# Optimization experiments

Measured on AMD Instinct MI355X. Metric: run time of the kernel, lower is better.

## Reference

```python
import jax, jax.numpy as jnp
import numpy as np

N = 50000      # nodes
E = 800000     # edges (avg degree 16)
CIN = 64       # in_channels
COUT = 128     # hidden_channels (block out_channels)
TC = 512       # time_channels = 4*hidden
H = 4          # attention heads
DH = COUT // H # head dim
G = 8          # group-norm groups
SLOPE = 0.01   # LeakyReLU default slope


def group_norm(x, w, b, groups=G, eps=1e-5):
    n, c = x.shape
    xg = x.reshape(n, groups, c // groups)
    mu = xg.mean(-1, keepdims=True)
    var = xg.var(-1, keepdims=True)
    xn = ((xg - mu) * jax.lax.rsqrt(var + eps)).reshape(n, c)
    return xn * w + b


def gcn_conv(x, W, b, row, col, ew, n):
    # GCNConv: add self loops (weight 1), symmetric normalization
    sl = jnp.arange(n)
    r = jnp.concatenate([row, sl])
    c = jnp.concatenate([col, sl])
    w2 = jnp.concatenate([ew, jnp.ones((n,), ew.dtype)])
    deg = jax.ops.segment_sum(w2, c, num_segments=n)
    dinv = jnp.where(deg > 0, jax.lax.rsqrt(deg), 0.0)
    norm = dinv[r] * w2 * dinv[c]            # [E+N]
    xw = x @ W                                # [N, Cout]
    out = jax.ops.segment_sum(norm[:, None] * xw[r], c, num_segments=n)
    return out + b


def gat_conv(x, Wa, a_src, a_dst, a_edge, ba, row, col, ew, n):
    # GAT-style attention conv; self-loop edge weight filled with max(edge_weight)
    sl = jnp.arange(n)
    fill = ew.max()
    r = jnp.concatenate([row, sl])
    c = jnp.concatenate([col, sl])
    w2 = jnp.concatenate([ew, jnp.full((n,), fill, ew.dtype)])
    h = (x @ Wa).reshape(n, H, DH)            # [N, H, DH]
    al_s = (h * a_src).sum(-1)                # [N, H]
    al_d = (h * a_dst).sum(-1)                # [N, H]
    logits = jax.nn.leaky_relu(al_s[r] + al_d[c] + a_edge * w2[:, None], 0.2)
    m = jax.ops.segment_max(logits, c, num_segments=n)
    e = jnp.exp(logits - m[c])
    s = jax.ops.segment_sum(e, c, num_segments=n)
    alpha = e / (s[c] + 1e-16)                # [E+N, H]
    out = jax.ops.segment_sum(alpha[:, :, None] * h[r], c, num_segments=n)
    return out.reshape(n, H * DH) + ba


def setup_inputs() -> dict:
    key = jax.random.key(0)
    ks = jax.random.split(key, 24)
    def w(k, shape, fan_in):
        return (jax.random.normal(k, shape, jnp.float32) / np.sqrt(fan_in)).astype(jnp.float32)
    inp = {
        "x": jax.random.normal(ks[0], (N, CIN), jnp.float32),
        "t": jax.random.normal(ks[1], (TC,), jnp.float32),
        "edge_index": jax.random.randint(ks[2], (2, E), 0, N, jnp.int32),
        "edge_weight": jax.random.uniform(ks[3], (E,), jnp.float32),
        # ResBlock norm/conv params
        "gn0_w": jnp.ones((CIN,), jnp.float32), "gn0_b": jnp.zeros((CIN,), jnp.float32),
        "W1": w(ks[4], (CIN, COUT), CIN), "b1": jnp.zeros((COUT,), jnp.float32),
        "gn1_w": jnp.ones((COUT,), jnp.float32), "gn1_b": jnp.zeros((COUT,), jnp.float32),
        "W2": w(ks[5], (COUT, COUT), COUT), "b2": jnp.zeros((COUT,), jnp.float32),
        "Wres": w(ks[6], (CIN, COUT), CIN),
        "te_w": w(ks[7], (TC, COUT), TC), "te_b": jnp.zeros((COUT,), jnp.float32),
        # AttnBlock params
        "gn2_w": jnp.ones((COUT,), jnp.float32), "gn2_b": jnp.zeros((COUT,), jnp.float32),
        "Wa": w(ks[8], (COUT, H * DH), COUT),
        "a_src": w(ks[9], (H, DH), DH), "a_dst": w(ks[10], (H, DH), DH),
        "a_edge": w(ks[11], (H,), 1), "ba": jnp.zeros((H * DH,), jnp.float32),
    }
    return inp


def reference(x, t, edge_index, edge_weight,
              gn0_w, gn0_b, W1, b1, gn1_w, gn1_b, W2, b2, Wres, te_w, te_b,
              gn2_w, gn2_b, Wa, a_src, a_dst, a_edge, ba):
    row, col = edge_index[0], edge_index[1]
    leaky = lambda z: jax.nn.leaky_relu(z, SLOPE)
    # ResBlock (n_layers=2)
    h = gcn_conv(leaky(group_norm(x, gn0_w, gn0_b)), W1, b1, row, col, edge_weight, N)
    tt = leaky(t) @ te_w + te_b               # time embed, broadcasts over nodes
    h = h + tt
    h = gcn_conv(leaky(group_norm(h, gn1_w, gn1_b)), W2, b2, row, col, edge_weight, N)
    h = h + x @ Wres                          # residual (Cin != Cout -> Linear)
    # AttnBlock (n_layers=1)
    a = leaky(group_norm(h, gn2_w, gn2_b))
    out = gat_conv(a, Wa, a_src, a_dst, a_edge, ba, row, col, edge_weight, N)
    return out
```

## Files before the change

### kernel.cpp

```cpp
#include <hip/hip_runtime.h>
#include <math.h>

#define ELLW 48
#define FB 4

typedef __attribute__((ext_vector_type(8))) short frag_ab;
typedef __attribute__((ext_vector_type(4))) float frag_cd;

__device__ __forceinline__ float lk(float v, float s) { return v > 0.f ? v : v * s; }
__device__ __forceinline__ unsigned short f2b(float f) {
    unsigned u = __float_as_uint(f);
    return (unsigned short)((u + 0x7fffu + ((u >> 16) & 1u)) >> 16);
}
__device__ __forceinline__ float b2f(unsigned h) { return __uint_as_float(h << 16); }

__global__ __launch_bounds__(256) void k_init(int* cnt, float* tt,
                                              const float* __restrict__ te_b,
                                              const float* __restrict__ b1, int n) {
    int i = blockIdx.x * 256 + threadIdx.x;
    if (i < n) cnt[i] = 0;
    if (i < 128) tt[i] = te_b[i] + b1[i];
}

__global__ __launch_bounds__(256) void k_fill_ell(const int* __restrict__ row,
                                                  const int* __restrict__ col,
                                                  const float* __restrict__ ew,
                                                  int* cnt, int2* __restrict__ ell,
                                                  float* __restrict__ bmax, int E) {
    int base = blockIdx.x * (256 * FB);
    int tid = threadIdx.x;
    int r[FB], c[FB]; float w[FB]; bool v[FB];
#pragma unroll
    for (int i = 0; i < FB; ++i) {
        int e = base + i * 256 + tid;
        v[i] = (e < E);
        r[i] = 0; c[i] = 0; w[i] = 0.f;
        if (v[i]) { r[i] = row[e]; c[i] = col[e]; w[i] = ew[e]; }
    }
    int pos[FB];
#pragma unroll
    for (int i = 0; i < FB; ++i)
        if (v[i]) pos[i] = atomicAdd(&cnt[c[i]], 1);
#pragma unroll
    for (int i = 0; i < FB; ++i)
        if (v[i] && pos[i] < ELLW)
            ell[(size_t)c[i] * ELLW + pos[i]] = make_int2(r[i], __float_as_int(w[i]));
    float m = 0.f;
#pragma unroll
    for (int i = 0; i < FB; ++i) m = fmaxf(m, w[i]);
    for (int o = 32; o; o >>= 1) m = fmaxf(m, __shfl_down(m, o, 64));
    __shared__ float sm[4];
    if ((tid & 63) == 0) sm[tid >> 6] = m;
    __syncthreads();
    if (tid == 0) bmax[blockIdx.x] = fmaxf(fmaxf(sm[0], sm[1]), fmaxf(sm[2], sm[3]));
}

__global__ __launch_bounds__(256) void k_ewmax_final(const float* __restrict__ bmax,
                                                     float* __restrict__ fill, int nb) {
    int tid = threadIdx.x;
    float m = 0.f;
    for (int i = tid; i < nb; i += 256) m = fmaxf(m, bmax[i]);
    for (int o = 32; o; o >>= 1) m = fmaxf(m, __shfl_down(m, o, 64));
    __shared__ float sm[4];
    if ((tid & 63) == 0) sm[tid >> 6] = m;
    __syncthreads();
    if (tid == 0) *fill = fmaxf(fmaxf(sm[0], sm[1]), fmaxf(sm[2], sm[3]));
}

__global__ __launch_bounds__(256) void k_node_deg(const int* __restrict__ cnt,
                                                  const int2* __restrict__ ell,
                                                  float* __restrict__ dinv, int n) {
    int i = blockIdx.x * 256 + threadIdx.x;
    if (i >= n) return;
    int c = min(cnt[i], ELLW);
    const int2* p = ell + (size_t)i * ELLW;
    float s = 1.f;
    for (int j = 0; j < c; ++j) s += __int_as_float(p[j].y);
    dinv[i] = rsqrtf(s);
}

__global__ __launch_bounds__(128) void k_tt(const float* __restrict__ t,
                                            const float* __restrict__ te_w, float* tt) {
    int co = threadIdx.x;
    int k0 = blockIdx.x * 32;
    float s = 0.f;
    for (int k = k0; k < k0 + 32; ++k) {
        float tv = t[k]; tv = tv > 0.f ? tv : 0.01f * tv;
        s = fmaf(tv, te_w[k * 128 + co], s);
    }
    unsafeAtomicAdd(&tt[co], s);
}

template <int K>
__global__ __launch_bounds__(256) void k_repack(const float* __restrict__ W, unsigned short* __restrict__ Wp) {
    int i = blockIdx.x * 256 + threadIdx.x;
    if (i >= K * 128) return;
    int k = i >> 7, nn = i & 127;
    int kc = k >> 5, quad = (k >> 3) & 3, j = k & 7;
    Wp[(((size_t)(kc * 4 + quad) * 128) + nn) * 8 + j] = f2b(W[i]);
}

template <int C>
__global__ __launch_bounds__(256) void k_gn(const float* __restrict__ in,
                                            const float* __restrict__ gw,
                                            const float* __restrict__ gb,
                                            unsigned short* __restrict__ outh,
                                            unsigned short* __restrict__ rawh, int n) {
    constexpr int CPG = C / 8;
    int gid = blockIdx.x * 256 + threadIdx.x;
    int row = gid >> 3, g = gid & 7;
    if (row >= n) return;
    const float* p = in + (size_t)row * C + g * CPG;
    float v[CPG];
#pragma unroll
    for (int j = 0; j < CPG; j += 4) {
        float4 t4 = *(const float4*)(p + j);
        v[j] = t4.x; v[j + 1] = t4.y; v[j + 2] = t4.z; v[j + 3] = t4.w;
    }
    float s = 0.f, s2 = 0.f;
#pragma unroll
    for (int j = 0; j < CPG; ++j) { s += v[j]; s2 += v[j] * v[j]; }
    float mu = s * (1.0f / CPG);
    float var = s2 * (1.0f / CPG) - mu * mu;
    float rstd = rsqrtf(var + 1e-5f);
    const float* wj = gw + g * CPG;
    const float* bj = gb + g * CPG;
    unsigned pk[CPG / 2];
#pragma unroll
    for (int j = 0; j < CPG; j += 2) {
        float y0 = lk((v[j + 0] - mu) * rstd * wj[j + 0] + bj[j + 0], 0.01f);
        float y1 = lk((v[j + 1] - mu) * rstd * wj[j + 1] + bj[j + 1], 0.01f);
        pk[j / 2] = (unsigned)f2b(y0) | ((unsigned)f2b(y1) << 16);
    }
    unsigned* q = (unsigned*)(outh + (size_t)row * C + g * CPG);
#pragma unroll
    for (int j = 0; j < CPG / 2; j += 4) *(uint4*)(q + j) = *(uint4*)(pk + j);
    if (rawh) {
#pragma unroll
        for (int j = 0; j < CPG; j += 2)
            pk[j / 2] = (unsigned)f2b(v[j]) | ((unsigned)f2b(v[j + 1]) << 16);
        unsigned* q2 = (unsigned*)(rawh + (size_t)row * C + g * CPG);
#pragma unroll
        for (int j = 0; j < CPG / 2; j += 4) *(uint4*)(q2 + j) = *(uint4*)(pk + j);
    }
}

template <int K>
__global__ __launch_bounds__(256) void k_mgemm(const unsigned short* __restrict__ Xh,
                                               const unsigned short* __restrict__ Wp,
                                               unsigned short* __restrict__ OUTh, int n) {
    int tid = threadIdx.x;
    int wave = tid >> 6, lane = tid & 63;
    int quad = lane >> 4, l16 = lane & 15;
    int rbase = blockIdx.x * 64 + wave * 16;
    int arow = rbase + l16; if (arow >= n) arow = n - 1;
    frag_cd acc[8];
#pragma unroll
    for (int t = 0; t < 8; ++t) acc[t] = (frag_cd){0.f, 0.f, 0.f, 0.f};
    const unsigned short* ap = Xh + (size_t)arow * K + quad * 8;
#pragma unroll
    for (int kc = 0; kc < K / 32; ++kc) {
        frag_ab a = *(const frag_ab*)(ap + kc * 32);
        const unsigned short* bp = Wp + ((size_t)(kc * 4 + quad) * 128 + l16) * 8;
#pragma unroll
        for (int t = 0; t < 8; ++t) {
            frag_ab b = *(const frag_ab*)(bp + (size_t)t * 128);
            acc[t] = __builtin_amdgcn_mfma_f32_16x16x32_bf16(a, b, acc[t], 0, 0, 0);
        }
    }
#pragma unroll
    for (int reg = 0; reg < 4; ++reg) {
        int r = rbase + quad * 4 + reg;
        if (r >= n) continue;
#pragma unroll
        for (int t = 0; t < 8; ++t)
            OUTh[(size_t)r * 128 + t * 16 + l16] = f2b(acc[t][reg]);
    }
}

__global__ __launch_bounds__(256) void k_mgemm2(const unsigned short* __restrict__ X1,
                                                const unsigned short* __restrict__ W2p,
                                                const unsigned short* __restrict__ X2,
                                                const unsigned short* __restrict__ Wrp,
                                                unsigned short* __restrict__ OUTh,
                                                float* __restrict__ C2,
                                                const float* __restrict__ bias, int n) {
    int tid = threadIdx.x;
    int wave = tid >> 6, lane = tid & 63;
    int quad = lane >> 4, l16 = lane & 15;
    int rbase = blockIdx.x * 64 + wave * 16;
    int arow = rbase + l16; if (arow >= n) arow = n - 1;
    frag_cd acc1[8], acc2[8];
#pragma unroll
    for (int t = 0; t < 8; ++t) {
        acc1[t] = (frag_cd){0.f, 0.f, 0.f, 0.f};
        acc2[t] = (frag_cd){0.f, 0.f, 0.f, 0.f};
    }
    const unsigned short* ap1 = X1 + (size_t)arow * 128 + quad * 8;
#pragma unroll
    for (int kc = 0; kc < 4; ++kc) {
        frag_ab a = *(const frag_ab*)(ap1 + kc * 32);
        const unsigned short* bp = W2p + ((size_t)(kc * 4 + quad) * 128 + l16) * 8;
#pragma unroll
        for (int t = 0; t < 8; ++t) {
            frag_ab b = *(const frag_ab*)(bp + (size_t)t * 128);
            acc1[t] = __builtin_amdgcn_mfma_f32_16x16x32_bf16(a, b, acc1[t], 0, 0, 0);
        }
    }
    const unsigned short* ap2 = X2 + (size_t)arow * 64 + quad * 8;
#pragma unroll
    for (int kc = 0; kc < 2; ++kc) {
        frag_ab a = *(const frag_ab*)(ap2 + kc * 32);
        const unsigned short* bp = Wrp + ((size_t)(kc * 4 + quad) * 128 + l16) * 8;
#pragma unroll
        for (int t = 0; t < 8; ++t) {
            frag_ab b = *(const frag_ab*)(bp + (size_t)t * 128);
            acc2[t] = __builtin_amdgcn_mfma_f32_16x16x32_bf16(a, b, acc2[t], 0, 0, 0);
        }
    }
#pragma unroll
    for (int reg = 0; reg < 4; ++reg) {
        int r = rbase + quad * 4 + reg;
        if (r >= n) continue;
#pragma unroll
        for (int t = 0; t < 8; ++t) {
            int c = t * 16 + l16;
            size_t o = (size_t)r * 128 + c;
            OUTh[o] = f2b(acc1[t][reg]);
            C2[o] = bias[c] + acc2[t][reg];
        }
    }
}

template <int BASEVEC>
__global__ __launch_bounds__(256) void k_gather_gn(const int* __restrict__ cnt,
                                                   const int2* __restrict__ ell,
                                                   const float* __restrict__ dinv,
                                                   const unsigned short* __restrict__ Bh,
                                                   const float* __restrict__ basevec,
                                                   const float* __restrict__ basebuf,
                                                   const float* __restrict__ gw,
                                                   const float* __restrict__ gb,
                                                   unsigned short* __restrict__ outh, int n) {
    int gid = blockIdx.x * 256 + threadIdx.x;
    int node = gid >> 5, q = gid & 31;
    if (node >= n) return;
    int s = node * ELLW;
    int e2 = s + min(cnt[node], ELLW);
    float a0 = 0.f, a1 = 0.f, a2 = 0.f, a3 = 0.f;
    int j = s;
    for (; j + 4 <= e2; j += 4) {
        int2 p0 = ell[j], p1 = ell[j + 1], p2 = ell[j + 2], p3 = ell[j + 3];
        float d0 = dinv[p0.x], d1 = dinv[p1.x], d2 = dinv[p2.x], d3 = dinv[p3.x];
        uint2 v0 = *(const uint2*)(Bh + (size_t)p0.x * 128 + q * 4);
        uint2 v1 = *(const uint2*)(Bh + (size_t)p1.x * 128 + q * 4);
        uint2 v2 = *(const uint2*)(Bh + (size_t)p2.x * 128 + q * 4);
        uint2 v3 = *(const uint2*)(Bh + (size_t)p3.x * 128 + q * 4);
        float w0 = d0 * __int_as_float(p0.y), w1 = d1 * __int_as_float(p1.y);
        float w2 = d2 * __int_as_float(p2.y), w3 = d3 * __int_as_float(p3.y);
        a0 = fmaf(w0, b2f(v0.x & 0xffffu), a0); a1 = fmaf(w0, b2f(v0.x >> 16), a1);
        a2 = fmaf(w0, b2f(v0.y & 0xffffu), a2); a3 = fmaf(w0, b2f(v0.y >> 16), a3);
        a0 = fmaf(w1, b2f(v1.x & 0xffffu), a0); a1 = fmaf(w1, b2f(v1.x >> 16), a1);
        a2 = fmaf(w1, b2f(v1.y & 0xffffu), a2); a3 = fmaf(w1, b2f(v1.y >> 16), a3);
        a0 = fmaf(w2, b2f(v2.x & 0xffffu), a0); a1 = fmaf(w2, b2f(v2.x >> 16), a1);
        a2 = fmaf(w2, b2f(v2.y & 0xffffu), a2); a3 = fmaf(w2, b2f(v2.y >> 16), a3);
        a0 = fmaf(w3, b2f(v3.x & 0xffffu), a0); a1 = fmaf(w3, b2f(v3.x >> 16), a1);
        a2 = fmaf(w3, b2f(v3.y & 0xffffu), a2); a3 = fmaf(w3, b2f(v3.y >> 16), a3);
    }
    for (; j < e2; ++j) {
        int2 p = ell[j];
        float nw = dinv[p.x] * __int_as_float(p.y);
        uint2 hv = *(const uint2*)(Bh + (size_t)p.x * 128 + q * 4);
        a0 = fmaf(nw, b2f(hv.x & 0xffffu), a0);
        a1 = fmaf(nw, b2f(hv.x >> 16), a1);
        a2 = fmaf(nw, b2f(hv.y & 0xffffu), a2);
        a3 = fmaf(nw, b2f(hv.y >> 16), a3);
    }
    float dc = dinv[node];
    uint2 sv = *(const uint2*)(Bh + (size_t)node * 128 + q * 4);
    a0 = dc * fmaf(dc, b2f(sv.x & 0xffffu), a0);
    a1 = dc * fmaf(dc, b2f(sv.x >> 16), a1);
    a2 = dc * fmaf(dc, b2f(sv.y & 0xffffu), a2);
    a3 = dc * fmaf(dc, b2f(sv.y >> 16), a3);
    float h0, h1, h2, h3;
    if constexpr (BASEVEC) {
        float4 bb = *(const float4*)(basevec + q * 4);
        h0 = bb.x + a0; h1 = bb.y + a1; h2 = bb.z + a2; h3 = bb.w + a3;
    } else {
        float4 bb = *(const float4*)(basebuf + (size_t)node * 128 + q * 4);
        h0 = bb.x + a0; h1 = bb.y + a1; h2 = bb.z + a2; h3 = bb.w + a3;
    }
    float sum = (h0 + h1) + (h2 + h3);
    float sq = fmaf(h0, h0, fmaf(h1, h1, fmaf(h2, h2, h3 * h3)));
    sum += __shfl_xor(sum, 1, 64); sum += __shfl_xor(sum, 2, 64);
    sq  += __shfl_xor(sq, 1, 64);  sq  += __shfl_xor(sq, 2, 64);
    float mu = sum * (1.0f / 16.0f);
    float var = sq * (1.0f / 16.0f) - mu * mu;
    float rstd = rsqrtf(var + 1e-5f);
    float4 gwv = *(const float4*)(gw + q * 4);
    float4 gbv = *(const float4*)(gb + q * 4);
    float y0 = lk((h0 - mu) * rstd * gwv.x + gbv.x, 0.01f);
    float y1 = lk((h1 - mu) * rstd * gwv.y + gbv.y, 0.01f);
    float y2 = lk((h2 - mu) * rstd * gwv.z + gbv.z, 0.01f);
    float y3 = lk((h3 - mu) * rstd * gwv.w + gbv.w, 0.01f);
    uint2 o;
    o.x = (unsigned)f2b(y0) | ((unsigned)f2b(y1) << 16);
    o.y = (unsigned)f2b(y2) | ((unsigned)f2b(y3) << 16);
    *(uint2*)(outh + (size_t)node * 128 + q * 4) = o;
}

__global__ __launch_bounds__(256) void k_al(const unsigned short* __restrict__ HAh,
                                            const float* __restrict__ a_src,
                                            const float* __restrict__ a_dst,
                                            float* __restrict__ als, float* __restrict__ ald, int n) {
    int gid = blockIdx.x * 256 + threadIdx.x;
    if (gid >= n * 4) return;
    int row = gid >> 2, hd = gid & 3;
    const unsigned* p = (const unsigned*)(HAh + (size_t)row * 128 + hd * 32);
    float ss = 0.f, sd = 0.f;
#pragma unroll
    for (int j = 0; j < 16; ++j) {
        unsigned u = p[j];
        float f0 = b2f(u & 0xffffu), f1 = b2f(u >> 16);
        float s0 = a_src[hd * 32 + j * 2], s1 = a_src[hd * 32 + j * 2 + 1];
        float d0 = a_dst[hd * 32 + j * 2], d1 = a_dst[hd * 32 + j * 2 + 1];
        ss = fmaf(f0, s0, fmaf(f1, s1, ss));
        sd = fmaf(f0, d0, fmaf(f1, d1, sd));
    }
    als[gid] = ss; ald[gid] = sd;
}

__global__ __launch_bounds__(256) void k_gat_gather(const int* __restrict__ cnt,
                                                    const int2* __restrict__ ell,
                                                    const float* __restrict__ als,
                                                    const float* __restrict__ ald,
                                                    const float* __restrict__ a_edge,
                                                    const float* __restrict__ fill,
                                                    const unsigned short* __restrict__ HAh,
                                                    const float* __restrict__ ba,
                                                    float* __restrict__ out, int n) {
    int gid = blockIdx.x * 256 + threadIdx.x;
    int node = gid >> 5, q = gid & 31, hd = q >> 3;
    if (node >= n) return;
    int s = node * ELLW;
    int e2 = s + min(cnt[node], ELLW);
    float ae = a_edge[hd];
    float aldc = ald[node * 4 + hd];
    float wself = *fill;
    float pself = __expf(lk(als[node * 4 + hd] + aldc + ae * wself, 0.2f));
    float den = pself;
    uint2 hv = *(const uint2*)(HAh + (size_t)node * 128 + q * 4);
    float a0 = pself * b2f(hv.x & 0xffffu), a1 = pself * b2f(hv.x >> 16);
    float a2 = pself * b2f(hv.y & 0xffffu), a3 = pself * b2f(hv.y >> 16);
    int j = s;
    for (; j + 4 <= e2; j += 4) {
        int2 p0 = ell[j], p1 = ell[j + 1], p2 = ell[j + 2], p3 = ell[j + 3];
        float s0 = als[p0.x * 4 + hd], s1 = als[p1.x * 4 + hd];
        float s2 = als[p2.x * 4 + hd], s3 = als[p3.x * 4 + hd];
        uint2 v0 = *(const uint2*)(HAh + (size_t)p0.x * 128 + q * 4);
        uint2 v1 = *(const uint2*)(HAh + (size_t)p1.x * 128 + q * 4);
        uint2 v2 = *(const uint2*)(HAh + (size_t)p2.x * 128 + q * 4);
        uint2 v3 = *(const uint2*)(HAh + (size_t)p3.x * 128 + q * 4);
        float pe0 = __expf(lk(s0 + aldc + ae * __int_as_float(p0.y), 0.2f));
        float pe1 = __expf(lk(s1 + aldc + ae * __int_as_float(p1.y), 0.2f));
        float pe2 = __expf(lk(s2 + aldc + ae * __int_as_float(p2.y), 0.2f));
        float pe3 = __expf(lk(s3 + aldc + ae * __int_as_float(p3.y), 0.2f));
        den += (pe0 + pe1) + (pe2 + pe3);
        a0 = fmaf(pe0, b2f(v0.x & 0xffffu), a0); a1 = fmaf(pe0, b2f(v0.x >> 16), a1);
        a2 = fmaf(pe0, b2f(v0.y & 0xffffu), a2); a3 = fmaf(pe0, b2f(v0.y >> 16), a3);
        a0 = fmaf(pe1, b2f(v1.x & 0xffffu), a0); a1 = fmaf(pe1, b2f(v1.x >> 16), a1);
        a2 = fmaf(pe1, b2f(v1.y & 0xffffu), a2); a3 = fmaf(pe1, b2f(v1.y >> 16), a3);
        a0 = fmaf(pe2, b2f(v2.x & 0xffffu), a0); a1 = fmaf(pe2, b2f(v2.x >> 16), a1);
        a2 = fmaf(pe2, b2f(v2.y & 0xffffu), a2); a3 = fmaf(pe2, b2f(v2.y >> 16), a3);
        a0 = fmaf(pe3, b2f(v3.x & 0xffffu), a0); a1 = fmaf(pe3, b2f(v3.x >> 16), a1);
        a2 = fmaf(pe3, b2f(v3.y & 0xffffu), a2); a3 = fmaf(pe3, b2f(v3.y >> 16), a3);
    }
    for (; j < e2; ++j) {
        int2 p = ell[j];
        float pe = __expf(lk(als[p.x * 4 + hd] + aldc + ae * __int_as_float(p.y), 0.2f));
        den += pe;
        uint2 v = *(const uint2*)(HAh + (size_t)p.x * 128 + q * 4);
        a0 = fmaf(pe, b2f(v.x & 0xffffu), a0);
        a1 = fmaf(pe, b2f(v.x >> 16), a1);
        a2 = fmaf(pe, b2f(v.y & 0xffffu), a2);
        a3 = fmaf(pe, b2f(v.y >> 16), a3);
    }
    float inv = 1.0f / (den + 1e-16f);
    const float* bb = ba + q * 4;
    float4 o;
    o.x = bb[0] + a0 * inv; o.y = bb[1] + a1 * inv;
    o.z = bb[2] + a2 * inv; o.w = bb[3] + a3 * inv;
    *(float4*)&out[(size_t)node * 128 + q * 4] = o;
}

extern "C" void kernel_launch(void* const* d_in, const int* in_sizes, int n_in,
                              void* d_out, int out_size, void* d_ws, size_t ws_size,
                              hipStream_t stream) {
    const float* x     = (const float*)d_in[0];
    const float* t     = (const float*)d_in[1];
    const int*   eidx  = (const int*)d_in[2];
    const float* ew    = (const float*)d_in[3];
    const float* gn0_w = (const float*)d_in[4];
    const float* gn0_b = (const float*)d_in[5];
    const float* W1    = (const float*)d_in[6];
    const float* b1    = (const float*)d_in[7];
    const float* gn1_w = (const float*)d_in[8];
    const float* gn1_b = (const float*)d_in[9];
    const float* W2    = (const float*)d_in[10];
    const float* b2    = (const float*)d_in[11];
    const float* Wres  = (const float*)d_in[12];
    const float* te_w  = (const float*)d_in[13];
    const float* te_b  = (const float*)d_in[14];
    const float* gn2_w = (const float*)d_in[15];
    const float* gn2_b = (const float*)d_in[16];
    const float* Wa    = (const float*)d_in[17];
    const float* a_src = (const float*)d_in[18];
    const float* a_dst = (const float*)d_in[19];
    const float* a_edge= (const float*)d_in[20];
    const float* ba    = (const float*)d_in[21];

    int n = in_sizes[0] / 64;
    int E = in_sizes[3];
    const int* rowp = eidx;
    const int* colp = eidx + E;

    char* p = (char*)d_ws;
    float* fC = (float*)p;                 p += (size_t)n * 128 * 4;
    unsigned short* fDh = (unsigned short*)p; p += (size_t)n * 128 * 2;
    unsigned short* fBh = (unsigned short*)p; p += (size_t)n * 128 * 2;
    unsigned short* xh  = (unsigned short*)p; p += (size_t)n * 64 * 2;
    int2* ell = (int2*)p;                  p += (size_t)n * ELLW * 8;
    unsigned short* W1p   = (unsigned short*)p; p += 64 * 128 * 2;
    unsigned short* W2p   = (unsigned short*)p; p += 128 * 128 * 2;
    unsigned short* Wap   = (unsigned short*)p; p += 128 * 128 * 2;
    unsigned short* Wresp = (unsigned short*)p; p += 64 * 128 * 2;
    float* dinv = (float*)p;               p += (size_t)n * 4;
    float* tt  = (float*)p;                p += 128 * 4;
    float* fill = (float*)p;               p += 16;
    float* als = (float*)p;                p += (size_t)4 * n * 4;
    float* ald = (float*)p;                p += (size_t)4 * n * 4;
    int* cnt    = (int*)p;                 p += (size_t)n * 4;
    float* bmax = (float*)p;               p += 4096 * 4;
    float* out = (float*)d_out;

    auto cdiv = [](long long a, long long b) { return (int)((a + b - 1) / b); };
    int nbf = cdiv(E, 256 * FB);

    k_init<<<cdiv(n, 256), 256, 0, stream>>>(cnt, tt, te_b, b1, n);
    k_fill_ell<<<nbf, 256, 0, stream>>>(rowp, colp, ew, cnt, ell, bmax, E);
    k_ewmax_final<<<1, 256, 0, stream>>>(bmax, fill, nbf);
    k_node_deg<<<cdiv(n, 256), 256, 0, stream>>>(cnt, ell, dinv, n);
    k_tt<<<16, 128, 0, stream>>>(t, te_w, tt);
    k_repack<64><<<cdiv(64 * 128, 256), 256, 0, stream>>>(W1, W1p);
    k_repack<128><<<cdiv(128 * 128, 256), 256, 0, stream>>>(W2, W2p);
    k_repack<128><<<cdiv(128 * 128, 256), 256, 0, stream>>>(Wa, Wap);
    k_repack<64><<<cdiv(64 * 128, 256), 256, 0, stream>>>(Wres, Wresp);

    k_gn<64><<<cdiv(8LL * n, 256), 256, 0, stream>>>(x, gn0_w, gn0_b, fDh, xh, n);
    k_mgemm<64><<<cdiv(n, 64), 256, 0, stream>>>(fDh, W1p, fBh, n);
    k_gather_gn<1><<<cdiv(32LL * n, 256), 256, 0, stream>>>(cnt, ell, dinv, fBh, tt, nullptr,
                                                            gn1_w, gn1_b, fDh, n);

    k_mgemm2<<<cdiv(n, 64), 256, 0, stream>>>(fDh, W2p, xh, Wresp, fBh, fC, b2, n);
    k_gather_gn<0><<<cdiv(32LL * n, 256), 256, 0, stream>>>(cnt, ell, dinv, fBh, nullptr, fC,
                                                            gn2_w, gn2_b, fDh, n);

    k_mgemm<128><<<cdiv(n, 64), 256, 0, stream>>>(fDh, Wap, fBh, n);
    k_al<<<cdiv(4LL * n, 256), 256, 0, stream>>>(fBh, a_src, a_dst, als, ald, n);
    k_gat_gather<<<cdiv(32LL * n, 256), 256, 0, stream>>>(cnt, ell, als, ald, a_edge, fill, fBh, ba, out, n);
}
```

Measured before the change: 341.9 us.

## Pack ELL entries into 32 bits and pre-scale GEMM outputs by dinv

Each ELL entry is shrunk from an int2 to one 32-bit word holding a 16-bit source index and a bf16 edge weight. This halves adjacency traffic and allows uint4 loads of four edges. The source-side dinv factor is folded into the GEMM epilogue, so the gathers no longer do a random dinv lookup per edge. Small setup kernels are merged to cut launches. The 16-bit index only holds for node counts up to 65536, and rounding edge weights to bf16 loses precision in the degree, norm and attention logits.

```diff
diff --git a/kernel.cpp b/kernel.cpp
--- a/kernel.cpp
+++ b/kernel.cpp
@@ -25,7 +25,7 @@
 __global__ __launch_bounds__(256) void k_fill_ell(const int* __restrict__ row,
                                                   const int* __restrict__ col,
                                                   const float* __restrict__ ew,
-                                                  int* cnt, int2* __restrict__ ell,
+                                                  int* cnt, unsigned* __restrict__ ell,
                                                   float* __restrict__ bmax, int E) {
     int base = blockIdx.x * (256 * FB);
     int tid = threadIdx.x;
@@ -44,7 +44,7 @@
 #pragma unroll
     for (int i = 0; i < FB; ++i)
         if (v[i] && pos[i] < ELLW)
-            ell[(size_t)c[i] * ELLW + pos[i]] = make_int2(r[i], __float_as_int(w[i]));
+            ell[(size_t)c[i] * ELLW + pos[i]] = (unsigned)r[i] | ((unsigned)f2b(w[i]) << 16);
     float m = 0.f;
 #pragma unroll
     for (int i = 0; i < FB; ++i) m = fmaxf(m, w[i]);
@@ -55,28 +55,29 @@
     if (tid == 0) bmax[blockIdx.x] = fmaxf(fmaxf(sm[0], sm[1]), fmaxf(sm[2], sm[3]));
 }
 
-__global__ __launch_bounds__(256) void k_ewmax_final(const float* __restrict__ bmax,
-                                                     float* __restrict__ fill, int nb) {
+__global__ __launch_bounds__(256) void k_node_deg(const int* __restrict__ cnt,
+                                                  const unsigned* __restrict__ ell,
+                                                  float* __restrict__ dinv,
+                                                  const float* __restrict__ bmax,
+                                                  float* __restrict__ fill, int n, int nb) {
     int tid = threadIdx.x;
-    float m = 0.f;
-    for (int i = tid; i < nb; i += 256) m = fmaxf(m, bmax[i]);
-    for (int o = 32; o; o >>= 1) m = fmaxf(m, __shfl_down(m, o, 64));
-    __shared__ float sm[4];
-    if ((tid & 63) == 0) sm[tid >> 6] = m;
-    __syncthreads();
-    if (tid == 0) *fill = fmaxf(fmaxf(sm[0], sm[1]), fmaxf(sm[2], sm[3]));
-}
-
-__global__ __launch_bounds__(256) void k_node_deg(const int* __restrict__ cnt,
-                                                  const int2* __restrict__ ell,
-                                                  float* __restrict__ dinv, int n) {
-    int i = blockIdx.x * 256 + threadIdx.x;
-    if (i >= n) return;
-    int c = min(cnt[i], ELLW);
-    const int2* p = ell + (size_t)i * ELLW;
-    float s = 1.f;
-    for (int j = 0; j < c; ++j) s += __int_as_float(p[j].y);
-    dinv[i] = rsqrtf(s);
+    int i = blockIdx.x * 256 + tid;
+    if (i < n) {
+        int c = min(cnt[i], ELLW);
+        const unsigned* p = ell + (size_t)i * ELLW;
+        float s = 1.f;
+        for (int j = 0; j < c; ++j) s += b2f(p[j] >> 16);
+        dinv[i] = rsqrtf(s);
+    }
+    if (blockIdx.x == 0) {
+        float m = 0.f;
+        for (int k = tid; k < nb; k += 256) m = fmaxf(m, bmax[k]);
+        for (int o = 32; o; o >>= 1) m = fmaxf(m, __shfl_down(m, o, 64));
+        __shared__ float sm[4];
+        if ((tid & 63) == 0) sm[tid >> 6] = m;
+        __syncthreads();
+        if (tid == 0) *fill = fmaxf(fmaxf(sm[0], sm[1]), fmaxf(sm[2], sm[3]));
+    }
 }
 
 __global__ __launch_bounds__(128) void k_tt(const float* __restrict__ t,
@@ -92,12 +93,24 @@
 }
 
 template <int K>
-__global__ __launch_bounds__(256) void k_repack(const float* __restrict__ W, unsigned short* __restrict__ Wp) {
-    int i = blockIdx.x * 256 + threadIdx.x;
-    if (i >= K * 128) return;
+__device__ __forceinline__ void repack1(const float* __restrict__ W,
+                                        unsigned short* __restrict__ Wp, int i) {
     int k = i >> 7, nn = i & 127;
     int kc = k >> 5, quad = (k >> 3) & 3, j = k & 7;
     Wp[(((size_t)(kc * 4 + quad) * 128) + nn) * 8 + j] = f2b(W[i]);
+}
+
+__global__ __launch_bounds__(256) void k_repack_all(const float* __restrict__ W1,
+                                                    const float* __restrict__ W2,
+                                                    const float* __restrict__ Wa,
+                                                    const float* __restrict__ Wres,
+                                                    unsigned short* W1p, unsigned short* W2p,
+                                                    unsigned short* Wap, unsigned short* Wrp) {
+    int i = blockIdx.x * 256 + threadIdx.x;
+    if (i < 8192)        repack1<64>(W1, W1p, i);
+    else if (i < 24576)  repack1<128>(W2, W2p, i - 8192);
+    else if (i < 40960)  repack1<128>(Wa, Wap, i - 24576);
+    else if (i < 49152)  repack1<64>(Wres, Wrp, i - 40960);
 }
 
 template <int C>
@@ -145,10 +158,11 @@
     }
 }
 
-template <int K>
+template <int K, int SCALE>
 __global__ __launch_bounds__(256) void k_mgemm(const unsigned short* __restrict__ Xh,
                                                const unsigned short* __restrict__ Wp,
-                                               unsigned short* __restrict__ OUTh, int n) {
+                                               unsigned short* __restrict__ OUTh,
+                                               const float* __restrict__ dinv, int n) {
     int tid = threadIdx.x;
     int wave = tid >> 6, lane = tid & 63;
     int quad = lane >> 4, l16 = lane & 15;
@@ -172,9 +186,11 @@
     for (int reg = 0; reg < 4; ++reg) {
         int r = rbase + quad * 4 + reg;
         if (r >= n) continue;
+        float sc = 1.f;
+        if constexpr (SCALE) sc = dinv[r];
 #pragma unroll
         for (int t = 0; t < 8; ++t)
-            OUTh[(size_t)r * 128 + t * 16 + l16] = f2b(acc[t][reg]);
+            OUTh[(size_t)r * 128 + t * 16 + l16] = f2b(sc * acc[t][reg]);
     }
 }
 
@@ -184,7 +200,8 @@
                                                 const unsigned short* __restrict__ Wrp,
                                                 unsigned short* __restrict__ OUTh,
                                                 float* __restrict__ C2,
-                                                const float* __restrict__ bias, int n) {
+                                                const float* __restrict__ bias,
+                                                const float* __restrict__ dinv, int n) {
     int tid = threadIdx.x;
     int wave = tid >> 6, lane = tid & 63;
     int quad = lane >> 4, l16 = lane & 15;
@@ -222,11 +239,12 @@
     for (int reg = 0; reg < 4; ++reg) {
         int r = rbase + quad * 4 + reg;
         if (r >= n) continue;
+        float sc = dinv[r];
 #pragma unroll
         for (int t = 0; t < 8; ++t) {
             int c = t * 16 + l16;
             size_t o = (size_t)r * 128 + c;
-            OUTh[o] = f2b(acc1[t][reg]);
+            OUTh[o] = f2b(sc * acc1[t][reg]);
             C2[o] = bias[c] + acc2[t][reg];
         }
     }
@@ -234,7 +252,7 @@
 
 template <int BASEVEC>
 __global__ __launch_bounds__(256) void k_gather_gn(const int* __restrict__ cnt,
-                                                   const int2* __restrict__ ell,
+                                                   const unsigned* __restrict__ ell,
                                                    const float* __restrict__ dinv,
                                                    const unsigned short* __restrict__ Bh,
                                                    const float* __restrict__ basevec,
@@ -250,14 +268,14 @@
     float a0 = 0.f, a1 = 0.f, a2 = 0.f, a3 = 0.f;
     int j = s;
     for (; j + 4 <= e2; j += 4) {
-        int2 p0 = ell[j], p1 = ell[j + 1], p2 = ell[j + 2], p3 = ell[j + 3];
-        float d0 = dinv[p0.x], d1 = dinv[p1.x], d2 = dinv[p2.x], d3 = dinv[p3.x];
-        uint2 v0 = *(const uint2*)(Bh + (size_t)p0.x * 128 + q * 4);
-        uint2 v1 = *(const uint2*)(Bh + (size_t)p1.x * 128 + q * 4);
-        uint2 v2 = *(const uint2*)(Bh + (size_t)p2.x * 128 + q * 4);
-        uint2 v3 = *(const uint2*)(Bh + (size_t)p3.x * 128 + q * 4);
-        float w0 = d0 * __int_as_float(p0.y), w1 = d1 * __int_as_float(p1.y);
-        float w2 = d2 * __int_as_float(p2.y), w3 = d3 * __int_as_float(p3.y);
+        uint4 pe = *(const uint4*)(ell + j);
+        int r0 = pe.x & 0xffffu, r1 = pe.y & 0xffffu, r2 = pe.z & 0xffffu, r3 = pe.w & 0xffffu;
+        float w0 = b2f(pe.x >> 16), w1 = b2f(pe.y >> 16);
+        float w2 = b2f(pe.z >> 16), w3 = b2f(pe.w >> 16);
+        uint2 v0 = *(const uint2*)(Bh + (size_t)r0 * 128 + q * 4);
+        uint2 v1 = *(const uint2*)(Bh + (size_t)r1 * 128 + q * 4);
+        uint2 v2 = *(const uint2*)(Bh + (size_t)r2 * 128 + q * 4);
+        uint2 v3 = *(const uint2*)(Bh + (size_t)r3 * 128 + q * 4);
         a0 = fmaf(w0, b2f(v0.x & 0xffffu), a0); a1 = fmaf(w0, b2f(v0.x >> 16), a1);
         a2 = fmaf(w0, b2f(v0.y & 0xffffu), a2); a3 = fmaf(w0, b2f(v0.y >> 16), a3);
         a0 = fmaf(w1, b2f(v1.x & 0xffffu), a0); a1 = fmaf(w1, b2f(v1.x >> 16), a1);
@@ -268,9 +286,10 @@
         a2 = fmaf(w3, b2f(v3.y & 0xffffu), a2); a3 = fmaf(w3, b2f(v3.y >> 16), a3);
     }
     for (; j < e2; ++j) {
-        int2 p = ell[j];
-        float nw = dinv[p.x] * __int_as_float(p.y);
-        uint2 hv = *(const uint2*)(Bh + (size_t)p.x * 128 + q * 4);
+        unsigned pe = ell[j];
+        int r = pe & 0xffffu;
+        float nw = b2f(pe >> 16);
+        uint2 hv = *(const uint2*)(Bh + (size_t)r * 128 + q * 4);
         a0 = fmaf(nw, b2f(hv.x & 0xffffu), a0);
         a1 = fmaf(nw, b2f(hv.x >> 16), a1);
         a2 = fmaf(nw, b2f(hv.y & 0xffffu), a2);
@@ -278,10 +297,10 @@
     }
     float dc = dinv[node];
     uint2 sv = *(const uint2*)(Bh + (size_t)node * 128 + q * 4);
-    a0 = dc * fmaf(dc, b2f(sv.x & 0xffffu), a0);
-    a1 = dc * fmaf(dc, b2f(sv.x >> 16), a1);
-    a2 = dc * fmaf(dc, b2f(sv.y & 0xffffu), a2);
-    a3 = dc * fmaf(dc, b2f(sv.y >> 16), a3);
+    a0 = dc * (a0 + b2f(sv.x & 0xffffu));
+    a1 = dc * (a1 + b2f(sv.x >> 16));
+    a2 = dc * (a2 + b2f(sv.y & 0xffffu));
+    a3 = dc * (a3 + b2f(sv.y >> 16));
     float h0, h1, h2, h3;
     if constexpr (BASEVEC) {
         float4 bb = *(const float4*)(basevec + q * 4);
@@ -331,7 +350,7 @@
 }
 
 __global__ __launch_bounds__(256) void k_gat_gather(const int* __restrict__ cnt,
-                                                    const int2* __restrict__ ell,
+                                                    const unsigned* __restrict__ ell,
                                                     const float* __restrict__ als,
                                                     const float* __restrict__ ald,
                                                     const float* __restrict__ a_edge,
@@ -354,17 +373,20 @@
     float a2 = pself * b2f(hv.y & 0xffffu), a3 = pself * b2f(hv.y >> 16);
     int j = s;
     for (; j + 4 <= e2; j += 4) {
-        int2 p0 = ell[j], p1 = ell[j + 1], p2 = ell[j + 2], p3 = ell[j + 3];
-        float s0 = als[p0.x * 4 + hd], s1 = als[p1.x * 4 + hd];
-        float s2 = als[p2.x * 4 + hd], s3 = als[p3.x * 4 + hd];
-        uint2 v0 = *(const uint2*)(HAh + (size_t)p0.x * 128 + q * 4);
-        uint2 v1 = *(const uint2*)(HAh + (size_t)p1.x * 128 + q * 4);
-        uint2 v2 = *(const uint2*)(HAh + (size_t)p2.x * 128 + q * 4);
-        uint2 v3 = *(const uint2*)(HAh + (size_t)p3.x * 128 + q * 4);
-        float pe0 = __expf(lk(s0 + aldc + ae * __int_as_float(p0.y), 0.2f));
-        float pe1 = __expf(lk(s1 + aldc + ae * __int_as_float(p1.y), 0.2f));
-        float pe2 = __expf(lk(s2 + aldc + ae * __int_as_float(p2.y), 0.2f));
-        float pe3 = __expf(lk(s3 + aldc + ae * __int_as_float(p3.y), 0.2f));
+        uint4 pe = *(const uint4*)(ell + j);
+        int r0 = pe.x & 0xffffu, r1 = pe.y & 0xffffu, r2 = pe.z & 0xffffu, r3 = pe.w & 0xffffu;
+        float w0 = b2f(pe.x >> 16), w1 = b2f(pe.y >> 16);
+        float w2 = b2f(pe.z >> 16), w3 = b2f(pe.w >> 16);
+        float s0 = als[r0 * 4 + hd], s1 = als[r1 * 4 + hd];
+        float s2 = als[r2 * 4 + hd], s3 = als[r3 * 4 + hd];
+        uint2 v0 = *(const uint2*)(HAh + (size_t)r0 * 128 + q * 4);
+        uint2 v1 = *(const uint2*)(HAh + (size_t)r1 * 128 + q * 4);
+        uint2 v2 = *(const uint2*)(HAh + (size_t)r2 * 128 + q * 4);
+        uint2 v3 = *(const uint2*)(HAh + (size_t)r3 * 128 + q * 4);
+        float pe0 = __expf(lk(s0 + aldc + ae * w0, 0.2f));
+        float pe1 = __expf(lk(s1 + aldc + ae * w1, 0.2f));
+        float pe2 = __expf(lk(s2 + aldc + ae * w2, 0.2f));
+        float pe3 = __expf(lk(s3 + aldc + ae * w3, 0.2f));
         den += (pe0 + pe1) + (pe2 + pe3);
         a0 = fmaf(pe0, b2f(v0.x & 0xffffu), a0); a1 = fmaf(pe0, b2f(v0.x >> 16), a1);
         a2 = fmaf(pe0, b2f(v0.y & 0xffffu), a2); a3 = fmaf(pe0, b2f(v0.y >> 16), a3);
@@ -376,14 +398,16 @@
         a2 = fmaf(pe3, b2f(v3.y & 0xffffu), a2); a3 = fmaf(pe3, b2f(v3.y >> 16), a3);
     }
     for (; j < e2; ++j) {
-        int2 p = ell[j];
-        float pe = __expf(lk(als[p.x * 4 + hd] + aldc + ae * __int_as_float(p.y), 0.2f));
-        den += pe;
-        uint2 v = *(const uint2*)(HAh + (size_t)p.x * 128 + q * 4);
-        a0 = fmaf(pe, b2f(v.x & 0xffffu), a0);
-        a1 = fmaf(pe, b2f(v.x >> 16), a1);
-        a2 = fmaf(pe, b2f(v.y & 0xffffu), a2);
-        a3 = fmaf(pe, b2f(v.y >> 16), a3);
+        unsigned pe = ell[j];
+        int r = pe & 0xffffu;
+        float w = b2f(pe >> 16);
+        float pev = __expf(lk(als[r * 4 + hd] + aldc + ae * w, 0.2f));
+        den += pev;
+        uint2 v = *(const uint2*)(HAh + (size_t)r * 128 + q * 4);
+        a0 = fmaf(pev, b2f(v.x & 0xffffu), a0);
+        a1 = fmaf(pev, b2f(v.x >> 16), a1);
+        a2 = fmaf(pev, b2f(v.y & 0xffffu), a2);
+        a3 = fmaf(pev, b2f(v.y >> 16), a3);
     }
     float inv = 1.0f / (den + 1e-16f);
     const float* bb = ba + q * 4;
@@ -429,7 +453,7 @@
     unsigned short* fDh = (unsigned short*)p; p += (size_t)n * 128 * 2;
     unsigned short* fBh = (unsigned short*)p; p += (size_t)n * 128 * 2;
     unsigned short* xh  = (unsigned short*)p; p += (size_t)n * 64 * 2;
-    int2* ell = (int2*)p;                  p += (size_t)n * ELLW * 8;
+    unsigned* ell = (unsigned*)p;          p += (size_t)n * ELLW * 4;
     unsigned short* W1p   = (unsigned short*)p; p += 64 * 128 * 2;
     unsigned short* W2p   = (unsigned short*)p; p += 128 * 128 * 2;
     unsigned short* Wap   = (unsigned short*)p; p += 128 * 128 * 2;
@@ -448,24 +472,20 @@
 
     k_init<<<cdiv(n, 256), 256, 0, stream>>>(cnt, tt, te_b, b1, n);
     k_fill_ell<<<nbf, 256, 0, stream>>>(rowp, colp, ew, cnt, ell, bmax, E);
-    k_ewmax_final<<<1, 256, 0, stream>>>(bmax, fill, nbf);
-    k_node_deg<<<cdiv(n, 256), 256, 0, stream>>>(cnt, ell, dinv, n);
+    k_node_deg<<<cdiv(n, 256), 256, 0, stream>>>(cnt, ell, dinv, bmax, fill, n, nbf);
     k_tt<<<16, 128, 0, stream>>>(t, te_w, tt);
-    k_repack<64><<<cdiv(64 * 128, 256), 256, 0, stream>>>(W1, W1p);
-    k_repack<128><<<cdiv(128 * 128, 256), 256, 0, stream>>>(W2, W2p);
-    k_repack<128><<<cdiv(128 * 128, 256), 256, 0, stream>>>(Wa, Wap);
-    k_repack<64><<<cdiv(64 * 128, 256), 256, 0, stream>>>(Wres, Wresp);
+    k_repack_all<<<cdiv(49152, 256), 256, 0, stream>>>(W1, W2, Wa, Wres, W1p, W2p, Wap, Wresp);
 
     k_gn<64><<<cdiv(8LL * n, 256), 256, 0, stream>>>(x, gn0_w, gn0_b, fDh, xh, n);
-    k_mgemm<64><<<cdiv(n, 64), 256, 0, stream>>>(fDh, W1p, fBh, n);
+    k_mgemm<64, 1><<<cdiv(n, 64), 256, 0, stream>>>(fDh, W1p, fBh, dinv, n);
     k_gather_gn<1><<<cdiv(32LL * n, 256), 256, 0, stream>>>(cnt, ell, dinv, fBh, tt, nullptr,
                                                             gn1_w, gn1_b, fDh, n);
 
-    k_mgemm2<<<cdiv(n, 64), 256, 0, stream>>>(fDh, W2p, xh, Wresp, fBh, fC, b2, n);
+    k_mgemm2<<<cdiv(n, 64), 256, 0, stream>>>(fDh, W2p, xh, Wresp, fBh, fC, b2, dinv, n);
     k_gather_gn<0><<<cdiv(32LL * n, 256), 256, 0, stream>>>(cnt, ell, dinv, fBh, nullptr, fC,
                                                             gn2_w, gn2_b, fDh, n);
 
-    k_mgemm<128><<<cdiv(n, 64), 256, 0, stream>>>(fDh, Wap, fBh, n);
+    k_mgemm<128, 0><<<cdiv(n, 64), 256, 0, stream>>>(fDh, Wap, fBh, nullptr, n);
     k_al<<<cdiv(4LL * n, 256), 256, 0, stream>>>(fBh, a_src, a_dst, als, ald, n);
     k_gat_gather<<<cdiv(32LL * n, 256), 256, 0, stream>>>(cnt, ell, als, ald, a_edge, fill, fBh, ba, out, n);
 }
```

Result: faster. 326.3 us (-4.6%).
